# Performance work log

Measured on AMD Instinct MI355X. Metric: run time of the kernel, lower is better.

The kernel has to match this reference:

```python
import jax, jax.numpy as jnp
import numpy as np

NUM_HEADS = 12
DIM = 768


def setup_inputs() -> dict:
    key = jax.random.key(0)
    ks = jax.random.split(key, 7)
    B, S, E = 8, 1024, DIM
    s = 0.02
    return {
        "x": jax.random.normal(ks[0], (B, S, E), dtype=jnp.float32),
        "Wq": jax.random.normal(ks[1], (E, E), dtype=jnp.float32) * s,
        "bq": jnp.zeros((E,), dtype=jnp.float32),
        "Wk": jax.random.normal(ks[2], (E, E), dtype=jnp.float32) * s,
        "bk": jnp.zeros((E,), dtype=jnp.float32),
        "Wo": jax.random.normal(ks[3], (E, E), dtype=jnp.float32) * s,
        "bo": jnp.zeros((E,), dtype=jnp.float32),
    }


def reference(x, Wq, bq, Wk, bk, Wo, bo):
    B, S, E = x.shape
    n = NUM_HEADS
    d = E // n
    scale = d ** (-0.5)

    def heads(t):  # [B,S,E] -> [B,n,S,d]
        return t.reshape(B, S, n, d).transpose(0, 2, 1, 3)

    q = heads(x @ Wq.T + bq)
    k = heads(x @ Wk.T + bk)
    v = k  # faithful to source bug: v = self.k_w(x)

    attn = jnp.einsum('bnqd,bnkd->bnqk', q, k) * scale  # [B,n,S,S]
    attn = jax.nn.softmax(attn, axis=-1)
    out = jnp.einsum('bnqk,bnkd->bnqd', attn, v)  # [B,n,S,d]
    out = out.transpose(0, 2, 1, 3).reshape(B, S, E)
    return out @ Wo.T + bo
```

## Files before the change

kernel.cpp:

```cpp
#include <hip/hip_runtime.h>
#include <stdint.h>


using short8   = __attribute__((ext_vector_type(8))) short;
using float4v  = __attribute__((ext_vector_type(4))) float;
using float16v = __attribute__((ext_vector_type(16))) float;

struct __align__(8) U2 { unsigned x, y; };

__device__ __forceinline__ void async16(void* lds, const void* g) {
  __builtin_amdgcn_global_load_lds(
      (const __attribute__((address_space(1))) void*)g,
      (__attribute__((address_space(3))) void*)lds, 16, 0, 0);
}

__device__ __forceinline__ unsigned bf16b(float f) {
  union { float f; unsigned u; } v; v.f = f;
  unsigned r = v.u + 0x7FFFu + ((v.u >> 16) & 1u);
  return r >> 16;
}

__global__ __launch_bounds__(256) void cvt_bf16(const float* __restrict__ in,
                                                unsigned short* __restrict__ out,
                                                int n8) {
  int i = blockIdx.x * 256 + threadIdx.x;
  if (i >= n8) return;
  const float4v* p = (const float4v*)in;
  float4v a = p[i * 2], b = p[i * 2 + 1];
  short8 o;
  o[0] = (short)bf16b(a[0]); o[1] = (short)bf16b(a[1]);
  o[2] = (short)bf16b(a[2]); o[3] = (short)bf16b(a[3]);
  o[4] = (short)bf16b(b[0]); o[5] = (short)bf16b(b[1]);
  o[6] = (short)bf16b(b[2]); o[7] = (short)bf16b(b[3]);
  ((short8*)out)[i] = o;
}

template <int MODE>
__global__ __launch_bounds__(256) void gemm_bt(
    const unsigned short* __restrict__ A, const unsigned short* __restrict__ B,
    const int M, const int N, const int K,
    const float* __restrict__ bias0, const float* __restrict__ bias1,
    void* __restrict__ outa, void* __restrict__ outb, void* __restrict__ outc) {
  __shared__ __align__(16) unsigned short a_l[4096];
  __shared__ __align__(16) unsigned short b_l[4096];
  const int tid = threadIdx.x;
  const int w = tid >> 6, lane = tid & 63;
  const int Q4 = lane >> 4, r = lane & 15;
  const int m0 = blockIdx.y * 128;
  const int n0 = blockIdx.x * 128;
  const int wm = w >> 1, wn = w & 1;

  float4v acc[4][4];
#pragma unroll
  for (int i = 0; i < 4; ++i)
#pragma unroll
    for (int j = 0; j < 4; ++j)
#pragma unroll
      for (int g = 0; g < 4; ++g) acc[i][j][g] = 0.0f;

  const unsigned short* Ab = A + (size_t)m0 * K;
  const unsigned short* Bb = B + (size_t)n0 * K;

  for (int kt = 0; kt < K; kt += 32) {
    __syncthreads();
#pragma unroll
    for (int ci = 0; ci < 2; ++ci) {
      int c = w * 2 + ci;
      int row = c * 16 + r;
      async16(&a_l[c * 512 + lane * 8], Ab + (size_t)row * K + kt + Q4 * 8);
      async16(&b_l[c * 512 + lane * 8], Bb + (size_t)row * K + kt + Q4 * 8);
    }
    __syncthreads();

    short8 af[4], bf[4];
#pragma unroll
    for (int i = 0; i < 4; ++i) {
      af[i] = *(const short8*)&a_l[(wm * 4 + i) * 512 + lane * 8];
      bf[i] = *(const short8*)&b_l[(wn * 4 + i) * 512 + lane * 8];
    }
#pragma unroll
    for (int mt = 0; mt < 4; ++mt)
#pragma unroll
      for (int nt = 0; nt < 4; ++nt)
        acc[mt][nt] = __builtin_amdgcn_mfma_f32_16x16x32_bf16(
            af[mt], bf[nt], acc[mt][nt], 0, 0, 0);
  }

  if (MODE == 0) {
    const bool isq = (n0 < 768);
    const float* bias = isq ? bias0 : bias1;
    unsigned short* outp = (unsigned short*)(isq ? outa : outb);
    const int nb = isq ? n0 : (n0 - 768);
    const float scl = isq ? 0.125f : 1.0f;
#pragma unroll
    for (int nt = 0; nt < 4; ++nt) {
      int n = nb + wn * 64 + nt * 16 + r;
      float bv = bias[n];
#pragma unroll
      for (int mt = 0; mt < 4; ++mt) {
        int m = m0 + wm * 64 + mt * 16 + Q4 * 4;
#pragma unroll
        for (int g = 0; g < 4; ++g)
          outp[(size_t)(m + g) * 768 + n] = (unsigned short)bf16b((acc[mt][nt][g] + bv) * scl);
      }
    }
    if (!isq) {
      unsigned short* ktp = (unsigned short*)outc;
      const int bq = m0 >> 10;
      const int sbase = (m0 & 1023) + wm * 64 + (Q4 & 1) * 8 + (Q4 >> 1) * 4;
#pragma unroll
      for (int nt = 0; nt < 4; ++nt) {
        int n = nb + wn * 64 + nt * 16 + r;
        int hh = n >> 6, dd = n & 63;
        float bv = bias[n];
#pragma unroll
        for (int mt = 0; mt < 4; ++mt) {
          int ns = sbase + mt * 16;
          unsigned lo = bf16b(acc[mt][nt][0] + bv) | (bf16b(acc[mt][nt][1] + bv) << 16);
          unsigned hi = bf16b(acc[mt][nt][2] + bv) | (bf16b(acc[mt][nt][3] + bv) << 16);
          *(U2*)(ktp + (size_t)((bq * 12 + hh) * 64 + dd) * 1024 + ns) = U2{lo, hi};
        }
      }
    }
  } else {
    float* outp = (float*)outa;
#pragma unroll
    for (int nt = 0; nt < 4; ++nt) {
      int n = n0 + wn * 64 + nt * 16 + r;
      float bv = bias0[n];
#pragma unroll
      for (int mt = 0; mt < 4; ++mt) {
        int m = m0 + wm * 64 + mt * 16 + Q4 * 4;
#pragma unroll
        for (int g = 0; g < 4; ++g)
          outp[(size_t)(m + g) * (size_t)N + n] = acc[mt][nt][g] + bv;
      }
    }
  }
}

__global__ __launch_bounds__(256, 3) void attn_fused(
    const unsigned short* __restrict__ qg,
    const unsigned short* __restrict__ kg,
    const unsigned short* __restrict__ ktg,
    unsigned short* __restrict__ ao) {
  __shared__ __align__(16) unsigned short q_l[8192];
  __shared__ __align__(16) unsigned short k_l[8192];
  __shared__ __align__(16) unsigned short vt_l[8192];

  const int tid = threadIdx.x;
  const int w = tid >> 6, lane = tid & 63;
  const int l31 = lane & 31, hi = lane >> 5;
  const int bid = blockIdx.x;
  const int b = bid & 7;
  const int h = bid >> 6;
  const int qt = (bid >> 3) & 7;
  const int q0 = qt * 128;
  const int bh = b * 12 + h;

#pragma unroll
  for (int ci = 0; ci < 4; ++ci) {
    int c = w * 4 + ci;
    async16(&q_l[c * 512 + lane * 8],
            qg + ((size_t)(b * 1024 + q0 + (c >> 2) * 32 + l31) * 768 + h * 64 + (c & 3) * 16 + hi * 8));
    async16(&k_l[c * 512 + lane * 8],
            kg + ((size_t)(b * 1024 + (c >> 2) * 32 + l31) * 768 + h * 64 + (c & 3) * 16 + hi * 8));
    async16(&vt_l[c * 512 + lane * 8],
            ktg + ((size_t)(bh * 64 + (c >> 3) * 32 + l31) * 1024 + (c & 7) * 16 + hi * 8));
  }
  __syncthreads();

  short8 bfq[4];
#pragma unroll
  for (int kb = 0; kb < 4; ++kb)
    bfq[kb] = *(const short8*)&q_l[(w * 4 + kb) * 512 + lane * 8];

  float16v o_acc[2];
#pragma unroll
  for (int db = 0; db < 2; ++db)
#pragma unroll
    for (int e = 0; e < 16; ++e) o_acc[db][e] = 0.0f;
  float ps = 0.0f;

#pragma unroll 1
  for (int it = 0; it < 8; ++it) {
    if (it > 0) {
      const int s0 = it * 128;
      __syncthreads();
#pragma unroll
      for (int ci = 0; ci < 4; ++ci) {
        int c = w * 4 + ci;
        async16(&k_l[c * 512 + lane * 8],
                kg + ((size_t)(b * 1024 + s0 + (c >> 2) * 32 + l31) * 768 + h * 64 + (c & 3) * 16 + hi * 8));
        async16(&vt_l[c * 512 + lane * 8],
                ktg + ((size_t)(bh * 64 + (c >> 3) * 32 + l31) * 1024 + s0 + (c & 7) * 16 + hi * 8));
      }
      __syncthreads();
    }

    float16v sc[4];
#pragma unroll
    for (int sb = 0; sb < 4; ++sb)
#pragma unroll
      for (int e = 0; e < 16; ++e) sc[sb][e] = 0.0f;
#pragma unroll
    for (int sb = 0; sb < 4; ++sb)
#pragma unroll
      for (int kb = 0; kb < 4; ++kb) {
        short8 af = *(const short8*)&k_l[(sb * 4 + kb) * 512 + lane * 8];
        sc[sb] = __builtin_amdgcn_mfma_f32_32x32x16_bf16(af, bfq[kb], sc[sb], 0, 0, 0);
      }

#pragma unroll
    for (int sb = 0; sb < 4; ++sb) {
      float pe[16];
#pragma unroll
      for (int e = 0; e < 16; ++e) pe[e] = __expf(sc[sb][e]);
#pragma unroll
      for (int e = 0; e < 16; ++e) ps += pe[e];
      short8 pf0, pf1;
#pragma unroll
      for (int e = 0; e < 8; ++e) {
        pf0[e] = (short)bf16b(pe[e]);
        pf1[e] = (short)bf16b(pe[8 + e]);
      }
#pragma unroll
      for (int db = 0; db < 2; ++db) {
        short8 vf0 = *(const short8*)&vt_l[(db * 8 + sb * 2) * 512 + lane * 8];
        o_acc[db] = __builtin_amdgcn_mfma_f32_32x32x16_bf16(vf0, pf0, o_acc[db], 0, 0, 0);
        short8 vf1 = *(const short8*)&vt_l[(db * 8 + sb * 2 + 1) * 512 + lane * 8];
        o_acc[db] = __builtin_amdgcn_mfma_f32_32x32x16_bf16(vf1, pf1, o_acc[db], 0, 0, 0);
      }
    }
  }

  ps += __shfl_xor(ps, 32, 64);
  const float inv = 1.0f / ps;
  const size_t rowbase = (size_t)(b * 1024 + q0 + w * 32 + l31) * 768 + h * 64;
#pragma unroll
  for (int db = 0; db < 2; ++db)
#pragma unroll
    for (int qq = 0; qq < 4; ++qq) {
      float v0 = o_acc[db][qq * 4 + 0] * inv;
      float v1 = o_acc[db][qq * 4 + 1] * inv;
      float v2 = o_acc[db][qq * 4 + 2] * inv;
      float v3 = o_acc[db][qq * 4 + 3] * inv;
      unsigned lo = bf16b(v0) | (bf16b(v1) << 16);
      unsigned hh = bf16b(v2) | (bf16b(v3) << 16);
      *(U2*)(ao + rowbase + db * 32 + qq * 8 + hi * 4) = U2{lo, hh};
    }
}

extern "C" void kernel_launch(void* const* d_in, const int* in_sizes, int n_in,
                              void* d_out, int out_size, void* d_ws, size_t ws_size,
                              hipStream_t stream) {
  const float* x  = (const float*)d_in[0];
  const float* Wq = (const float*)d_in[1];
  const float* bq = (const float*)d_in[2];
  const float* Wk = (const float*)d_in[3];
  const float* bk = (const float*)d_in[4];
  const float* Wo = (const float*)d_in[5];
  const float* bo = (const float*)d_in[6];
  (void)in_sizes; (void)n_in; (void)out_size; (void)ws_size;

  char* ws = (char*)d_ws;
  unsigned short* x_b   = (unsigned short*)(ws);
  unsigned short* wqk_b = (unsigned short*)(ws + 12582912);
  unsigned short* wo_b  = (unsigned short*)(ws + 14942208);
  unsigned short* q_b   = (unsigned short*)(ws + 16121856);
  unsigned short* k_b   = (unsigned short*)(ws + 28704768);
  unsigned short* kt_b  = (unsigned short*)(ws + 41287680);
  unsigned short* ao_b  = (unsigned short*)(ws + 53870592);

  cvt_bf16<<<3072, 256, 0, stream>>>(x, x_b, 786432);
  cvt_bf16<<<288, 256, 0, stream>>>(Wq, wqk_b, 73728);
  cvt_bf16<<<288, 256, 0, stream>>>(Wk, wqk_b + 589824, 73728);
  cvt_bf16<<<288, 256, 0, stream>>>(Wo, wo_b, 73728);

  gemm_bt<0><<<dim3(12, 64), 256, 0, stream>>>(x_b, wqk_b, 8192, 1536, 768,
                                               bq, bk, q_b, k_b, kt_b);
  attn_fused<<<768, 256, 0, stream>>>(q_b, k_b, kt_b, ao_b);
  gemm_bt<1><<<dim3(6, 64), 256, 0, stream>>>(ao_b, wo_b, 8192, 768, 768,
                                              bo, nullptr, d_out, nullptr, nullptr);
}
```

Baseline: 221.0 us.

## Specialize GEMMs with K=64 tiles, merge weight casts, use exp2 softmax

The templated GEMM is split into two specialized kernels. The QK projection now stages 64-wide K slices per barrier, and the output projection uses 64-row M tiles, which doubles its grid for better CU occupancy. The three weight conversion launches are merged into one kernel. The Q scale is folded into a log2(e) factor so the softmax can use exp2f in place of __expf. These changes cut barrier count and launch overhead at the cost of more LDS per block.

```diff
diff --git a/kernel.cpp b/kernel.cpp
--- a/kernel.cpp
+++ b/kernel.cpp
@@ -35,14 +35,33 @@
   ((short8*)out)[i] = o;
 }
 
-template <int MODE>
-__global__ __launch_bounds__(256) void gemm_bt(
+__global__ __launch_bounds__(256) void cvt_w3(const float* __restrict__ w0,
+                                              const float* __restrict__ w1,
+                                              const float* __restrict__ w2,
+                                              unsigned short* __restrict__ o0,
+                                              unsigned short* __restrict__ o1,
+                                              unsigned short* __restrict__ o2) {
+  int mi = blockIdx.x / 288;
+  int i = (blockIdx.x - mi * 288) * 256 + threadIdx.x;
+  const float* in = (mi == 0) ? w0 : (mi == 1) ? w1 : w2;
+  unsigned short* out = (mi == 0) ? o0 : (mi == 1) ? o1 : o2;
+  const float4v* p = (const float4v*)in;
+  float4v a = p[i * 2], b = p[i * 2 + 1];
+  short8 o;
+  o[0] = (short)bf16b(a[0]); o[1] = (short)bf16b(a[1]);
+  o[2] = (short)bf16b(a[2]); o[3] = (short)bf16b(a[3]);
+  o[4] = (short)bf16b(b[0]); o[5] = (short)bf16b(b[1]);
+  o[6] = (short)bf16b(b[2]); o[7] = (short)bf16b(b[3]);
+  ((short8*)out)[i] = o;
+}
+
+__global__ __launch_bounds__(256, 3) void sgemm_qk(
     const unsigned short* __restrict__ A, const unsigned short* __restrict__ B,
-    const int M, const int N, const int K,
     const float* __restrict__ bias0, const float* __restrict__ bias1,
-    void* __restrict__ outa, void* __restrict__ outb, void* __restrict__ outc) {
-  __shared__ __align__(16) unsigned short a_l[4096];
-  __shared__ __align__(16) unsigned short b_l[4096];
+    unsigned short* __restrict__ outq, unsigned short* __restrict__ outk,
+    unsigned short* __restrict__ outkt) {
+  __shared__ __align__(16) unsigned short a_l[8192];
+  __shared__ __align__(16) unsigned short b_l[8192];
   const int tid = threadIdx.x;
   const int w = tid >> 6, lane = tid & 63;
   const int Q4 = lane >> 4, r = lane & 15;
@@ -58,83 +77,144 @@
 #pragma unroll
       for (int g = 0; g < 4; ++g) acc[i][j][g] = 0.0f;
 
-  const unsigned short* Ab = A + (size_t)m0 * K;
-  const unsigned short* Bb = B + (size_t)n0 * K;
-
-  for (int kt = 0; kt < K; kt += 32) {
+  const unsigned short* Ab = A + (size_t)(m0 + r) * 768 + Q4 * 8;
+  const unsigned short* Bb = B + (size_t)(n0 + r) * 768 + Q4 * 8;
+
+  for (int kt = 0; kt < 768; kt += 64) {
     __syncthreads();
 #pragma unroll
-    for (int ci = 0; ci < 2; ++ci) {
-      int c = w * 2 + ci;
-      int row = c * 16 + r;
-      async16(&a_l[c * 512 + lane * 8], Ab + (size_t)row * K + kt + Q4 * 8);
-      async16(&b_l[c * 512 + lane * 8], Bb + (size_t)row * K + kt + Q4 * 8);
+    for (int ci = 0; ci < 4; ++ci) {
+      int idx = w * 4 + ci;
+      int c = idx >> 1, kh = idx & 1;
+      async16(&a_l[idx * 512 + lane * 8], Ab + c * 16 * 768 + kt + kh * 32);
+      async16(&b_l[idx * 512 + lane * 8], Bb + c * 16 * 768 + kt + kh * 32);
     }
     __syncthreads();
 
-    short8 af[4], bf[4];
-#pragma unroll
-    for (int i = 0; i < 4; ++i) {
-      af[i] = *(const short8*)&a_l[(wm * 4 + i) * 512 + lane * 8];
-      bf[i] = *(const short8*)&b_l[(wn * 4 + i) * 512 + lane * 8];
-    }
+    short8 af[4][2], bf[4][2];
+#pragma unroll
+    for (int i = 0; i < 4; ++i)
+#pragma unroll
+      for (int ks = 0; ks < 2; ++ks) {
+        af[i][ks] = *(const short8*)&a_l[((wm * 4 + i) * 2 + ks) * 512 + lane * 8];
+        bf[i][ks] = *(const short8*)&b_l[((wn * 4 + i) * 2 + ks) * 512 + lane * 8];
+      }
 #pragma unroll
     for (int mt = 0; mt < 4; ++mt)
 #pragma unroll
       for (int nt = 0; nt < 4; ++nt)
-        acc[mt][nt] = __builtin_amdgcn_mfma_f32_16x16x32_bf16(
-            af[mt], bf[nt], acc[mt][nt], 0, 0, 0);
-  }
-
-  if (MODE == 0) {
-    const bool isq = (n0 < 768);
-    const float* bias = isq ? bias0 : bias1;
-    unsigned short* outp = (unsigned short*)(isq ? outa : outb);
-    const int nb = isq ? n0 : (n0 - 768);
-    const float scl = isq ? 0.125f : 1.0f;
+#pragma unroll
+        for (int ks = 0; ks < 2; ++ks)
+          acc[mt][nt] = __builtin_amdgcn_mfma_f32_16x16x32_bf16(
+              af[mt][ks], bf[nt][ks], acc[mt][nt], 0, 0, 0);
+  }
+
+  const bool isq = (n0 < 768);
+  const float* bias = isq ? bias0 : bias1;
+  unsigned short* outp = isq ? outq : outk;
+  const int nb = isq ? n0 : (n0 - 768);
+  const float scl = isq ? 0.18033688011112042f : 1.0f;
+#pragma unroll
+  for (int nt = 0; nt < 4; ++nt) {
+    int n = nb + wn * 64 + nt * 16 + r;
+    float bv = bias[n];
+#pragma unroll
+    for (int mt = 0; mt < 4; ++mt) {
+      int m = m0 + wm * 64 + mt * 16 + Q4 * 4;
+#pragma unroll
+      for (int g = 0; g < 4; ++g)
+        outp[(size_t)(m + g) * 768 + n] = (unsigned short)bf16b((acc[mt][nt][g] + bv) * scl);
+    }
+  }
+  if (!isq) {
+    const int bq = m0 >> 10;
+    const int sbase = (m0 & 1023) + wm * 64 + (Q4 & 1) * 8 + (Q4 >> 1) * 4;
 #pragma unroll
     for (int nt = 0; nt < 4; ++nt) {
       int n = nb + wn * 64 + nt * 16 + r;
+      int hh = n >> 6, dd = n & 63;
       float bv = bias[n];
 #pragma unroll
       for (int mt = 0; mt < 4; ++mt) {
-        int m = m0 + wm * 64 + mt * 16 + Q4 * 4;
-#pragma unroll
-        for (int g = 0; g < 4; ++g)
-          outp[(size_t)(m + g) * 768 + n] = (unsigned short)bf16b((acc[mt][nt][g] + bv) * scl);
-      }
-    }
-    if (!isq) {
-      unsigned short* ktp = (unsigned short*)outc;
-      const int bq = m0 >> 10;
-      const int sbase = (m0 & 1023) + wm * 64 + (Q4 & 1) * 8 + (Q4 >> 1) * 4;
-#pragma unroll
-      for (int nt = 0; nt < 4; ++nt) {
-        int n = nb + wn * 64 + nt * 16 + r;
-        int hh = n >> 6, dd = n & 63;
-        float bv = bias[n];
-#pragma unroll
-        for (int mt = 0; mt < 4; ++mt) {
-          int ns = sbase + mt * 16;
-          unsigned lo = bf16b(acc[mt][nt][0] + bv) | (bf16b(acc[mt][nt][1] + bv) << 16);
-          unsigned hi = bf16b(acc[mt][nt][2] + bv) | (bf16b(acc[mt][nt][3] + bv) << 16);
-          *(U2*)(ktp + (size_t)((bq * 12 + hh) * 64 + dd) * 1024 + ns) = U2{lo, hi};
-        }
-      }
-    }
-  } else {
-    float* outp = (float*)outa;
-#pragma unroll
-    for (int nt = 0; nt < 4; ++nt) {
-      int n = n0 + wn * 64 + nt * 16 + r;
-      float bv = bias0[n];
-#pragma unroll
-      for (int mt = 0; mt < 4; ++mt) {
-        int m = m0 + wm * 64 + mt * 16 + Q4 * 4;
-#pragma unroll
-        for (int g = 0; g < 4; ++g)
-          outp[(size_t)(m + g) * (size_t)N + n] = acc[mt][nt][g] + bv;
-      }
+        int ns = sbase + mt * 16;
+        unsigned lo = bf16b(acc[mt][nt][0] + bv) | (bf16b(acc[mt][nt][1] + bv) << 16);
+        unsigned hi = bf16b(acc[mt][nt][2] + bv) | (bf16b(acc[mt][nt][3] + bv) << 16);
+        *(U2*)(outkt + (size_t)((bq * 12 + hh) * 64 + dd) * 1024 + ns) = U2{lo, hi};
+      }
+    }
+  }
+}
+
+__global__ __launch_bounds__(256, 3) void sgemm_out(
+    const unsigned short* __restrict__ A, const unsigned short* __restrict__ B,
+    const float* __restrict__ bias, float* __restrict__ outp) {
+  __shared__ __align__(16) unsigned short a_l[4096];
+  __shared__ __align__(16) unsigned short b_l[8192];
+  const int tid = threadIdx.x;
+  const int w = tid >> 6, lane = tid & 63;
+  const int Q4 = lane >> 4, r = lane & 15;
+  const int m0 = blockIdx.y * 64;
+  const int n0 = blockIdx.x * 128;
+  const int wm = w >> 1, wn = w & 1;
+
+  float4v acc[2][4];
+#pragma unroll
+  for (int i = 0; i < 2; ++i)
+#pragma unroll
+    for (int j = 0; j < 4; ++j)
+#pragma unroll
+      for (int g = 0; g < 4; ++g) acc[i][j][g] = 0.0f;
+
+  const unsigned short* Ab = A + (size_t)(m0 + r) * 768 + Q4 * 8;
+  const unsigned short* Bb = B + (size_t)(n0 + r) * 768 + Q4 * 8;
+
+  for (int kt = 0; kt < 768; kt += 64) {
+    __syncthreads();
+#pragma unroll
+    for (int ci = 0; ci < 2; ++ci) {
+      int idx = w * 2 + ci;
+      int c = idx >> 1, kh = idx & 1;
+      async16(&a_l[idx * 512 + lane * 8], Ab + c * 16 * 768 + kt + kh * 32);
+    }
+#pragma unroll
+    for (int ci = 0; ci < 4; ++ci) {
+      int idx = w * 4 + ci;
+      int c = idx >> 1, kh = idx & 1;
+      async16(&b_l[idx * 512 + lane * 8], Bb + c * 16 * 768 + kt + kh * 32);
+    }
+    __syncthreads();
+
+    short8 af[2][2], bf[4][2];
+#pragma unroll
+    for (int i = 0; i < 2; ++i)
+#pragma unroll
+      for (int ks = 0; ks < 2; ++ks)
+        af[i][ks] = *(const short8*)&a_l[((wm * 2 + i) * 2 + ks) * 512 + lane * 8];
+#pragma unroll
+    for (int i = 0; i < 4; ++i)
+#pragma unroll
+      for (int ks = 0; ks < 2; ++ks)
+        bf[i][ks] = *(const short8*)&b_l[((wn * 4 + i) * 2 + ks) * 512 + lane * 8];
+#pragma unroll
+    for (int mt = 0; mt < 2; ++mt)
+#pragma unroll
+      for (int nt = 0; nt < 4; ++nt)
+#pragma unroll
+        for (int ks = 0; ks < 2; ++ks)
+          acc[mt][nt] = __builtin_amdgcn_mfma_f32_16x16x32_bf16(
+              af[mt][ks], bf[nt][ks], acc[mt][nt], 0, 0, 0);
+  }
+
+#pragma unroll
+  for (int nt = 0; nt < 4; ++nt) {
+    int n = n0 + wn * 64 + nt * 16 + r;
+    float bv = bias[n];
+#pragma unroll
+    for (int mt = 0; mt < 2; ++mt) {
+      int m = m0 + wm * 32 + mt * 16 + Q4 * 4;
+#pragma unroll
+      for (int g = 0; g < 4; ++g)
+        outp[(size_t)(m + g) * 768 + n] = acc[mt][nt][g] + bv;
     }
   }
 }
@@ -215,7 +295,7 @@
     for (int sb = 0; sb < 4; ++sb) {
       float pe[16];
 #pragma unroll
-      for (int e = 0; e < 16; ++e) pe[e] = __expf(sc[sb][e]);
+      for (int e = 0; e < 16; ++e) pe[e] = exp2f(sc[sb][e]);
 #pragma unroll
       for (int e = 0; e < 16; ++e) ps += pe[e];
       short8 pf0, pf1;
@@ -273,13 +353,9 @@
   unsigned short* ao_b  = (unsigned short*)(ws + 53870592);
 
   cvt_bf16<<<3072, 256, 0, stream>>>(x, x_b, 786432);
-  cvt_bf16<<<288, 256, 0, stream>>>(Wq, wqk_b, 73728);
-  cvt_bf16<<<288, 256, 0, stream>>>(Wk, wqk_b + 589824, 73728);
-  cvt_bf16<<<288, 256, 0, stream>>>(Wo, wo_b, 73728);
-
-  gemm_bt<0><<<dim3(12, 64), 256, 0, stream>>>(x_b, wqk_b, 8192, 1536, 768,
-                                               bq, bk, q_b, k_b, kt_b);
+  cvt_w3<<<864, 256, 0, stream>>>(Wq, Wk, Wo, wqk_b, wqk_b + 589824, wo_b);
+
+  sgemm_qk<<<dim3(12, 64), 256, 0, stream>>>(x_b, wqk_b, bq, bk, q_b, k_b, kt_b);
   attn_fused<<<768, 256, 0, stream>>>(q_b, k_b, kt_b, ao_b);
-  gemm_bt<1><<<dim3(6, 64), 256, 0, stream>>>(ao_b, wo_b, 8192, 768, 768,
-                                              bo, nullptr, d_out, nullptr, nullptr);
-}
+  sgemm_out<<<dim3(6, 128), 256, 0, stream>>>(ao_b, wo_b, bo, (float*)d_out);
+}
```

New measurement: 216.5 us. 1.02x faster.
